# Kernel optimization log

Measured on AMD Instinct MI355X. Metric: run time of the kernel, lower is better.

## Reference

```python
import jax, jax.numpy as jnp
import numpy as np

T, B, F = 256, 256, 128   # seq_len, batch (graph nodes), feature_dim = graph_arch[0]
H1 = 256                  # graph_arch[1]
H = 128                   # graph_arch[-1] == lstm hidden_dim
Q = 4                     # n_qubits bottleneck per gate
TAGS = 32


def setup_inputs() -> dict:
    key = jax.random.key(0)
    ks = jax.random.split(key, 8)
    s = 0.05  # init scale for stability
    return {
        "node_sequences": jax.random.normal(ks[0], (T, B, F), jnp.float32),
        "adj": jax.random.uniform(ks[1], (B, B), jnp.float32),
        "W1": jax.random.normal(ks[2], (F, H1), jnp.float32) * s,
        "b1": jnp.zeros((H1,), jnp.float32),
        "W2": jax.random.normal(ks[3], (H1, H), jnp.float32) * s,
        "b2": jnp.zeros((H,), jnp.float32),
        "Win": jax.random.normal(ks[4], (4, F + H, Q), jnp.float32) * s,   # 4 gates: f,i,g,o
        "b_in": jnp.zeros((4, Q), jnp.float32),
        "Wout": jax.random.normal(ks[5], (4, Q, H), jnp.float32) * s,
        "b_out": jnp.zeros((4, H), jnp.float32),
        "Wtag": jax.random.normal(ks[6], (H, TAGS), jnp.float32) * s,
        "btag": jnp.zeros((TAGS,), jnp.float32),
    }


def reference(node_sequences, adj, W1, b1, W2, b2, Win, b_in, Wout, b_out, Wtag, btag):
    t, b, f = node_sequences.shape
    # per-node feedforward MLP (batched instead of the original per-sample loop)
    flat = node_sequences.reshape(t * b, f)
    a1 = jnp.tanh(flat @ W1 + b1)
    node_states = jnp.tanh(a1 @ W2 + b2).reshape(t, b, -1)   # [T,B,H]
    # fidelity-adjacency aggregation over the node (batch) axis
    aggregated = jnp.einsum('ij,tjf->tif', adj, node_states)  # [T,B,H]

    h_dim = Wout.shape[-1]

    def step(carry, x_t):
        h, c = carry
        v = jnp.concatenate([x_t, h], axis=-1)                       # [B, F+H]
        z = jnp.tanh(jnp.einsum('bv,gvq->gbq', v, Win) + b_in[:, None, :])   # quantum-layer bottleneck [4,B,Q]
        g = jnp.einsum('gbq,gqh->gbh', z, Wout) + b_out[:, None, :]          # [4,B,H]
        f_g = jax.nn.sigmoid(g[0])
        i_g = jax.nn.sigmoid(g[1])
        g_g = jnp.tanh(g[2])
        o_g = jax.nn.sigmoid(g[3])
        c = f_g * c + i_g * g_g
        h = o_g * jnp.tanh(c)
        return (h, c), h

    h0 = jnp.zeros((b, h_dim), node_sequences.dtype)
    c0 = jnp.zeros((b, h_dim), node_sequences.dtype)
    _, lstm_out = jax.lax.scan(step, (h0, c0), aggregated)   # [T,B,H]

    logits = lstm_out @ Wtag + btag                          # [T,B,TAGS]
    return jax.nn.log_softmax(logits, axis=2)
```

## Files before the change

### kernel.cpp

```cpp
#include <hip/hip_runtime.h>
#include <hip/hip_bf16.h>

#define T_DIM 256
#define B_DIM 256
#define F_DIM 128
#define H1_DIM 256
#define H_DIM 128
#define Q_DIM 4
#define TAGS 32
#define TB (T_DIM * B_DIM)

typedef __attribute__((ext_vector_type(8))) short bf16x8;
typedef __attribute__((ext_vector_type(4))) float f32x4;
typedef __attribute__((ext_vector_type(2))) float f32x2;

__device__ __forceinline__ float rcpf(float x) { return __builtin_amdgcn_rcpf(x); }
__device__ __forceinline__ float exp2f_hw(float x) { return __builtin_amdgcn_exp2f(x); }

__device__ __forceinline__ float tanhf_fast(float x) {
    float e = exp2f_hw(2.885390081777927f * x);
    return 1.0f - 2.0f * rcpf(e + 1.0f);
}
__device__ __forceinline__ float sigf(float x) {
    return rcpf(1.0f + exp2f_hw(-1.4426950408889634f * x));
}

__device__ __forceinline__ unsigned short f2bf(float f) {
    __hip_bfloat16 h = __float2bfloat16(f);
    return *reinterpret_cast<unsigned short*>(&h);
}

__device__ __forceinline__ f32x2 pk_mul2(f32x2 a, f32x2 b) {
    f32x2 d;
    asm("v_pk_mul_f32 %0, %1, %2" : "=v"(d) : "v"(a), "v"(b));
    return d;
}
__device__ __forceinline__ f32x2 pk_add2(f32x2 a, f32x2 b) {
    f32x2 d;
    asm("v_pk_add_f32 %0, %1, %2" : "=v"(d) : "v"(a), "v"(b));
    return d;
}
__device__ __forceinline__ f32x2 pk_fma2(f32x2 a, f32x2 b, f32x2 c) {
    f32x2 d;
    asm("v_pk_fma_f32 %0, %1, %2, %3" : "=v"(d) : "v"(a), "v"(b), "v"(c));
    return d;
}

template<int CTRL>
__device__ __forceinline__ float dpp_xadd(float x) {
    int t = __builtin_amdgcn_update_dpp(0, __float_as_int(x), CTRL, 0xF, 0xF, true);
    return x + __int_as_float(t);
}

__global__ __launch_bounds__(256) void prep_kernel(
    const float* __restrict__ W1, const float* __restrict__ W2,
    const float* __restrict__ Win, const float* __restrict__ Wtag,
    unsigned short* __restrict__ W1p, unsigned short* __restrict__ W2p,
    unsigned short* __restrict__ Winxp, unsigned short* __restrict__ Wtagp)
{
    const int gid0 = blockIdx.x * 256 + threadIdx.x;
    const int gstride = gridDim.x * 256;
    for (int idx = gid0; idx < 32768; idx += gstride) {
        int e = idx & 7, l = (idx >> 3) & 63, t2 = idx >> 9;
        int nb = t2 & 15, kk = t2 >> 4;
        int k = kk * 32 + (l >> 4) * 8 + e, n = nb * 16 + (l & 15);
        W1p[idx] = f2bf(W1[k * 256 + n]);
    }
    for (int idx = gid0; idx < 32768; idx += gstride) {
        int e = idx & 7, l = (idx >> 3) & 63, t2 = idx >> 9;
        int nb = t2 & 7, kk = t2 >> 3;
        int k = kk * 32 + (l >> 4) * 8 + e, n = nb * 16 + (l & 15);
        W2p[idx] = f2bf(W2[k * 128 + n]);
    }
    for (int idx = gid0; idx < 2048; idx += gstride) {
        int e = idx & 7, l = (idx >> 3) & 63, kk = idx >> 9;
        int k = kk * 32 + (l >> 4) * 8 + e, o = l & 15;
        Winxp[idx] = f2bf(Win[(o >> 2) * 1024 + k * 4 + (o & 3)]);
    }
    for (int idx = gid0; idx < 4096; idx += gstride) {
        int e = idx & 7, l = (idx >> 3) & 63, t2 = idx >> 9;
        int nt = t2 & 1, kk = t2 >> 1;
        int k = kk * 32 + (l >> 4) * 8 + e, n = nt * 16 + (l & 15);
        Wtagp[idx] = f2bf(Wtag[k * 32 + n]);
    }
}

__global__ __launch_bounds__(256) void mlp_mfma_kernel(
    const float* __restrict__ X, const unsigned short* __restrict__ W1p,
    const float* __restrict__ b1, const unsigned short* __restrict__ W2p,
    const float* __restrict__ b2, const unsigned short* __restrict__ Winxp,
    float* __restrict__ NSP)
{
    __shared__ __align__(16) unsigned short a1_s[64 * 256];
    __shared__ __align__(16) unsigned short xns_s[64 * 128];

    const int tid = threadIdx.x;
    const int w = tid >> 6;
    const int lane = tid & 63;
    const int lr = lane & 15;
    const int lg = lane >> 4;
    const long rowbase = (long)blockIdx.x * 64;

    char* const a1c = (char*)a1_s;
    char* const xnc = (char*)xns_s;

    {
        const int r = tid >> 2;
        const int qc = tid & 3;
        const float4* xg = (const float4*)(X + (rowbase + r) * 128 + qc * 32);
#pragma unroll
        for (int i = 0; i < 4; i++) {
            float4 lo = xg[i * 2], hi = xg[i * 2 + 1];
            bf16x8 v;
            v[0] = (short)f2bf(lo.x); v[1] = (short)f2bf(lo.y);
            v[2] = (short)f2bf(lo.z); v[3] = (short)f2bf(lo.w);
            v[4] = (short)f2bf(hi.x); v[5] = (short)f2bf(hi.y);
            v[6] = (short)f2bf(hi.z); v[7] = (short)f2bf(hi.w);
            int byte = (r * 256 + qc * 64 + i * 16) ^ ((r & 7) << 4);
            *(bf16x8*)(xnc + byte) = v;
        }
    }
    __syncthreads();

    {
        f32x4 acc[4][4];
#pragma unroll
        for (int mi = 0; mi < 4; mi++)
#pragma unroll
            for (int j = 0; j < 4; j++) acc[mi][j] = (f32x4){0.f, 0.f, 0.f, 0.f};

        const bf16x8* w1v = (const bf16x8*)W1p;
#pragma unroll
        for (int kk = 0; kk < 4; kk++) {
            bf16x8 af[4];
#pragma unroll
            for (int mi = 0; mi < 4; mi++) {
                int row = mi * 16 + lr;
                int byte = (row * 256 + kk * 64 + lg * 16) ^ ((row & 7) << 4);
                af[mi] = *(const bf16x8*)(xnc + byte);
            }
            bf16x8 bfv[4];
#pragma unroll
            for (int j = 0; j < 4; j++)
                bfv[j] = w1v[(kk * 16 + (w * 4 + j)) * 64 + lane];
#pragma unroll
            for (int mi = 0; mi < 4; mi++)
#pragma unroll
                for (int j = 0; j < 4; j++)
                    acc[mi][j] = __builtin_amdgcn_mfma_f32_16x16x32_bf16(
                        af[mi], bfv[j], acc[mi][j], 0, 0, 0);
        }

        float b1v[4];
#pragma unroll
        for (int j = 0; j < 4; j++) b1v[j] = b1[(w * 4 + j) * 16 + lr];
#pragma unroll
        for (int mi = 0; mi < 4; mi++)
#pragma unroll
            for (int j = 0; j < 4; j++)
#pragma unroll
                for (int reg = 0; reg < 4; reg++) {
                    int row = mi * 16 + lg * 4 + reg;
                    int col = (w * 4 + j) * 16 + lr;
                    float v = tanhf_fast(acc[mi][j][reg] + b1v[j]);
                    int byte = (row * 512 + col * 2) ^ ((row & 7) << 4);
                    *(unsigned short*)(a1c + byte) = f2bf(v);
                }
    }
    __syncthreads();

    {
        f32x4 acc[4][2];
#pragma unroll
        for (int mi = 0; mi < 4; mi++)
#pragma unroll
            for (int j = 0; j < 2; j++) acc[mi][j] = (f32x4){0.f, 0.f, 0.f, 0.f};

        const bf16x8* w2v = (const bf16x8*)W2p;
#pragma unroll
        for (int kk = 0; kk < 8; kk++) {
            bf16x8 af[4];
#pragma unroll
            for (int mi = 0; mi < 4; mi++) {
                int row = mi * 16 + lr;
                int byte = (row * 512 + kk * 64 + lg * 16) ^ ((row & 7) << 4);
                af[mi] = *(const bf16x8*)(a1c + byte);
            }
            bf16x8 bfv[2];
#pragma unroll
            for (int j = 0; j < 2; j++)
                bfv[j] = w2v[(kk * 8 + (w * 2 + j)) * 64 + lane];
#pragma unroll
            for (int mi = 0; mi < 4; mi++)
#pragma unroll
                for (int j = 0; j < 2; j++)
                    acc[mi][j] = __builtin_amdgcn_mfma_f32_16x16x32_bf16(
                        af[mi], bfv[j], acc[mi][j], 0, 0, 0);
        }

        float b2v[2];
#pragma unroll
        for (int j = 0; j < 2; j++) b2v[j] = b2[(w * 2 + j) * 16 + lr];
#pragma unroll
        for (int mi = 0; mi < 4; mi++)
#pragma unroll
            for (int j = 0; j < 2; j++)
#pragma unroll
                for (int reg = 0; reg < 4; reg++) {
                    int row = mi * 16 + lg * 4 + reg;
                    int col = (w * 2 + j) * 16 + lr;
                    float v = tanhf_fast(acc[mi][j][reg] + b2v[j]);
                    int byte = (row * 256 + col * 2) ^ ((row & 7) << 4);
                    *(unsigned short*)(xnc + byte) = f2bf(v);
                }
    }
    __syncthreads();

    {
        f32x4 acc = (f32x4){0.f, 0.f, 0.f, 0.f};
        const bf16x8* wxv = (const bf16x8*)Winxp;
#pragma unroll
        for (int kk = 0; kk < 4; kk++) {
            int row = w * 16 + lr;
            int byte = (row * 256 + kk * 64 + lg * 16) ^ ((row & 7) << 4);
            bf16x8 af = *(const bf16x8*)(xnc + byte);
            bf16x8 bfv = wxv[kk * 64 + lane];
            acc = __builtin_amdgcn_mfma_f32_16x16x32_bf16(af, bfv, acc, 0, 0, 0);
        }
#pragma unroll
        for (int reg = 0; reg < 4; reg++) {
            int row = w * 16 + lg * 4 + reg;
            NSP[(rowbase + row) * 16 + lr] = acc[reg];
        }
    }
}

__global__ __launch_bounds__(256) void transpose_kernel(
    const float* __restrict__ adj, float* __restrict__ adjT)
{
    __shared__ float tile[32][33];
    const int tid = threadIdx.x;
    const int bx = blockIdx.x & 7, by = blockIdx.x >> 3;
    const int lx = tid & 31, ly = (tid >> 5) * 4;
#pragma unroll
    for (int r = 0; r < 4; r++)
        tile[ly + r][lx] = adj[(long)(by * 32 + ly + r) * 256 + bx * 32 + lx];
    __syncthreads();
#pragma unroll
    for (int r = 0; r < 4; r++)
        adjT[(long)(bx * 32 + ly + r) * 256 + by * 32 + lx] = tile[lx][ly + r];
}

__global__ __launch_bounds__(256) void aggx_kernel(
    const float* __restrict__ adjT, const float* __restrict__ NSP,
    const float* __restrict__ b_in, float* __restrict__ AX)
{
    __shared__ float4 nsp_s[256 * 4];
    const int tid = threadIdx.x;
    const int t = blockIdx.x;
    {
        const float4* g = (const float4*)(NSP + (long)t * 4096);
#pragma unroll
        for (int i = 0; i < 4; i++) nsp_s[tid + i * 256] = g[tid + i * 256];
    }
    __syncthreads();

    float4 acc[4];
#pragma unroll
    for (int p = 0; p < 4; p++) acc[p] = ((const float4*)b_in)[p];

    const float* arow = adjT + tid;
    float a[8], an[8];
#pragma unroll
    for (int m = 0; m < 8; m++) an[m] = arow[m * 256];
    for (int j0 = 0; j0 < 256; j0 += 8) {
#pragma unroll
        for (int m = 0; m < 8; m++) a[m] = an[m];
        if (j0 + 8 < 256) {
#pragma unroll
            for (int m = 0; m < 8; m++) an[m] = arow[(j0 + 8 + m) * 256];
        }
#pragma unroll
        for (int m = 0; m < 8; m++) {
            float av = a[m];
#pragma unroll
            for (int p = 0; p < 4; p++) {
                float4 nv = nsp_s[(j0 + m) * 4 + p];
                acc[p].x += av * nv.x; acc[p].y += av * nv.y;
                acc[p].z += av * nv.z; acc[p].w += av * nv.w;
            }
        }
    }
    float4* out = (float4*)(AX + (long)t * 4096 + tid * 16);
#pragma unroll
    for (int p = 0; p < 4; p++) out[p] = acc[p];
}

__device__ __forceinline__ int hhoff(int row, int inrow) {
    return (row * 512 + inrow) ^ ((row & 7) << 4);
}

__global__ __attribute__((amdgpu_waves_per_eu(1, 1))) __launch_bounds__(64)
void lstm_head_kernel(
    const float* __restrict__ AX, const float* __restrict__ Win,
    const float* __restrict__ Wout, const float* __restrict__ b_out,
    const unsigned short* __restrict__ Wtagp, const float* __restrict__ btag,
    float* __restrict__ OUT)
{
    __shared__ __align__(16) float hh[T_DIM * 128];
    char* const hhc = (char*)hh;

    const int lane = threadIdx.x;
    const int b = blockIdx.x;
    const int o = lane >> 2;
    const int s = lane & 3;
    const int g_o = o >> 2, q_o = o & 3;

    f32x2 wh2[16];
#pragma unroll
    for (int m = 0; m < 8; m++)
#pragma unroll
        for (int p = 0; p < 2; p++) {
            int k0 = m * 16 + s * 4 + p * 2;
            f32x2 v;
            v.x = Win[g_o * 1024 + 512 + k0 * 4 + q_o];
            v.y = Win[g_o * 1024 + 512 + (k0 + 1) * 4 + q_o];
            wh2[m * 2 + p] = v;
        }

    float wo[4][4][2];
    float bo[4][2];
#pragma unroll
    for (int g = 0; g < 4; g++) {
#pragma unroll
        for (int h2 = 0; h2 < 2; h2++) bo[g][h2] = b_out[g * 128 + lane + 64 * h2];
#pragma unroll
        for (int q = 0; q < 4; q++)
#pragma unroll
            for (int h2 = 0; h2 < 2; h2++)
                wo[g][q][h2] = Wout[(g * 4 + q) * 128 + lane + 64 * h2];
    }

    int woffs[8], roffs[8];
#pragma unroll
    for (int sl = 0; sl < 8; sl++) {
        woffs[sl] = (lane * 4) ^ (sl << 4);
        roffs[sl] = (s * 16) ^ ((sl << 4) & 0x30);
    }

    float c0 = 0.f, c1 = 0.f;
    f32x2 hl[8], hx[8];
#pragma unroll
    for (int m = 0; m < 8; m++) { hl[m] = (f32x2){0.f, 0.f}; hx[m] = (f32x2){0.f, 0.f}; }

    const float* axp = AX + (long)b * 16 + o;
    float ax_cur = axp[0];
    float ax_nxt = axp[B_DIM * 16];
    axp += 2 * B_DIM * 16;

    int vbase = 0;
    for (int tb = 0; tb < T_DIM; tb += 8) {
#pragma unroll
        for (int sl = 0; sl < 8; sl++) {
            const int sw6 = (sl << 4) & 0x40;
            f32x2 aA = pk_mul2(hl[0], wh2[0]);
            f32x2 aB = pk_mul2(hl[1], wh2[1]);
            f32x2 aC = pk_mul2(hl[2], wh2[2]);
            f32x2 aD = pk_mul2(hl[3], wh2[3]);
            aA = pk_fma2(hl[4], wh2[4], aA);
            aB = pk_fma2(hl[5], wh2[5], aB);
            aC = pk_fma2(hl[6], wh2[6], aC);
            aD = pk_fma2(hl[7], wh2[7], aD);
            aA = pk_fma2(hx[0], wh2[8],  aA);
            aB = pk_fma2(hx[1], wh2[9],  aB);
            aC = pk_fma2(hx[2], wh2[10], aC);
            aD = pk_fma2(hx[3], wh2[11], aD);
            aA = pk_fma2(hx[4], wh2[12], aA);
            aB = pk_fma2(hx[5], wh2[13], aB);
            aC = pk_fma2(hx[6], wh2[14], aC);
            aD = pk_fma2(hx[7], wh2[15], aD);
            f32x2 sAB = pk_add2(aA, aB);
            f32x2 sCD = pk_add2(aC, aD);
            f32x2 sS  = pk_add2(sAB, sCD);
            float acc = sS.x + sS.y;
            acc = dpp_xadd<0xB1>(acc);
            acc = dpp_xadd<0x4E>(acc);
            float zv = tanhf_fast(acc + ax_cur);

            unsigned zb = __float_as_uint(zv);
            float z[16];
#pragma unroll
            for (int oo = 0; oo < 16; oo++)
                z[oo] = __uint_as_float(__builtin_amdgcn_readlane(zb, oo * 4));

            char* const wp = hhc + (vbase + woffs[sl]);
            const char* const rp = hhc + (vbase + roffs[sl]);

            {
                float gp_f = bo[0][0] + z[0]*wo[0][0][0] + z[1]*wo[0][1][0] + z[2]*wo[0][2][0] + z[3]*wo[0][3][0];
                float gp_i = bo[1][0] + z[4]*wo[1][0][0] + z[5]*wo[1][1][0] + z[6]*wo[1][2][0] + z[7]*wo[1][3][0];
                float gp_g = bo[2][0] + z[8]*wo[2][0][0] + z[9]*wo[2][1][0] + z[10]*wo[2][2][0] + z[11]*wo[2][3][0];
                float gp_o = bo[3][0] + z[12]*wo[3][0][0] + z[13]*wo[3][1][0] + z[14]*wo[3][2][0] + z[15]*wo[3][3][0];
                float fg = sigf(gp_f);
                float ig = sigf(gp_i);
                float gg = tanhf_fast(gp_g);
                float og = sigf(gp_o);
                c0 = fg * c0 + ig * gg;
                float h0 = og * tanhf_fast(c0);
                *(float*)(wp + sl * 512) = h0;
            }
#pragma unroll
            for (int m = 0; m < 4; m++) {
                hl[m * 2]     = *(const f32x2*)(rp + sl * 512 + ((m * 64) ^ sw6));
                hl[m * 2 + 1] = *(const f32x2*)(rp + sl * 512 + ((m * 64) ^ sw6) + 8);
            }

            {
                float gp_f = bo[0][1] + z[0]*wo[0][0][1] + z[1]*wo[0][1][1] + z[2]*wo[0][2][1] + z[3]*wo[0][3][1];
                float gp_i = bo[1][1] + z[4]*wo[1][0][1] + z[5]*wo[1][1][1] + z[6]*wo[1][2][1] + z[7]*wo[1][3][1];
                float gp_g = bo[2][1] + z[8]*wo[2][0][1] + z[9]*wo[2][1][1] + z[10]*wo[2][2][1] + z[11]*wo[2][3][1];
                float gp_o = bo[3][1] + z[12]*wo[3][0][1] + z[13]*wo[3][1][1] + z[14]*wo[3][2][1] + z[15]*wo[3][3][1];
                float fg = sigf(gp_f);
                float ig = sigf(gp_i);
                float gg = tanhf_fast(gp_g);
                float og = sigf(gp_o);
                c1 = fg * c1 + ig * gg;
                float h1 = og * tanhf_fast(c1);
                *(float*)(wp + sl * 512 + 256) = h1;
            }
#pragma unroll
            for (int m = 0; m < 4; m++) {
                hx[m * 2]     = *(const f32x2*)(rp + sl * 512 + 256 + ((m * 64) ^ sw6));
                hx[m * 2 + 1] = *(const f32x2*)(rp + sl * 512 + 256 + ((m * 64) ^ sw6) + 8);
            }

            ax_cur = ax_nxt;
            ax_nxt = *axp;
            axp += B_DIM * 16;
        }
        vbase += 8 * 512;
    }

    const int lr = lane & 15;
    const int lg = lane >> 4;
    const bf16x8* wtv = (const bf16x8*)Wtagp;
    bf16x8 wt[4][2];
#pragma unroll
    for (int kk = 0; kk < 4; kk++)
#pragma unroll
        for (int nt = 0; nt < 2; nt++)
            wt[kk][nt] = wtv[(kk * 2 + nt) * 64 + lane];
    float bt0 = btag[lr], bt1 = btag[16 + lr];

    for (int mi = 0; mi < 16; mi++) {
        f32x4 acc0 = (f32x4){0.f, 0.f, 0.f, 0.f};
        f32x4 acc1 = (f32x4){0.f, 0.f, 0.f, 0.f};
        const int arow = mi * 16 + lr;
#pragma unroll
        for (int kk = 0; kk < 4; kk++) {
            float4 lo = *(const float4*)(hhc + hhoff(arow, kk * 128 + lg * 32));
            float4 hi = *(const float4*)(hhc + hhoff(arow, kk * 128 + lg * 32 + 16));
            bf16x8 af;
            af[0] = (short)f2bf(lo.x); af[1] = (short)f2bf(lo.y);
            af[2] = (short)f2bf(lo.z); af[3] = (short)f2bf(lo.w);
            af[4] = (short)f2bf(hi.x); af[5] = (short)f2bf(hi.y);
            af[6] = (short)f2bf(hi.z); af[7] = (short)f2bf(hi.w);
            acc0 = __builtin_amdgcn_mfma_f32_16x16x32_bf16(af, wt[kk][0], acc0, 0, 0, 0);
            acc1 = __builtin_amdgcn_mfma_f32_16x16x32_bf16(af, wt[kk][1], acc1, 0, 0, 0);
        }
        float s0[4], s1[4], mx[4], se[4];
#pragma unroll
        for (int reg = 0; reg < 4; reg++) {
            s0[reg] = acc0[reg] + bt0;
            s1[reg] = acc1[reg] + bt1;
            float m = fmaxf(s0[reg], s1[reg]);
#pragma unroll
            for (int d = 8; d >= 1; d >>= 1) m = fmaxf(m, __shfl_xor(m, d));
            mx[reg] = m;
            float e = __expf(s0[reg] - m) + __expf(s1[reg] - m);
#pragma unroll
            for (int d = 8; d >= 1; d >>= 1) e += __shfl_xor(e, d);
            se[reg] = __logf(e);
        }
#pragma unroll
        for (int reg = 0; reg < 4; reg++) {
            long t = mi * 16 + lg * 4 + reg;
            long base = (t * B_DIM + b) * 32;
            OUT[base + lr]      = s0[reg] - mx[reg] - se[reg];
            OUT[base + 16 + lr] = s1[reg] - mx[reg] - se[reg];
        }
    }
}

extern "C" void kernel_launch(void* const* d_in, const int* in_sizes, int n_in,
                              void* d_out, int out_size, void* d_ws, size_t ws_size,
                              hipStream_t stream)
{
    const float* X    = (const float*)d_in[0];
    const float* adj  = (const float*)d_in[1];
    const float* W1   = (const float*)d_in[2];
    const float* b1   = (const float*)d_in[3];
    const float* W2   = (const float*)d_in[4];
    const float* b2   = (const float*)d_in[5];
    const float* Win  = (const float*)d_in[6];
    const float* b_in = (const float*)d_in[7];
    const float* Wout = (const float*)d_in[8];
    const float* bout = (const float*)d_in[9];
    const float* Wtag = (const float*)d_in[10];
    const float* btag = (const float*)d_in[11];
    float* OUT = (float*)d_out;

    float* ws = (float*)d_ws;
    float* NSP  = ws;
    float* adjT = ws + 1048576;
    float* AX   = ws + 1114112;
    unsigned short* W1p   = (unsigned short*)(ws + 2162688);
    unsigned short* W2p   = W1p + 32768;
    unsigned short* Winxp = W2p + 32768;
    unsigned short* Wtagp = Winxp + 2048;

    prep_kernel<<<dim3(64), dim3(256), 0, stream>>>(W1, W2, Win, Wtag, W1p, W2p, Winxp, Wtagp);
    mlp_mfma_kernel<<<dim3(TB / 64), dim3(256), 0, stream>>>(X, W1p, b1, W2p, b2, Winxp, NSP);
    transpose_kernel<<<dim3(64), dim3(256), 0, stream>>>(adj, adjT);
    aggx_kernel<<<dim3(256), dim3(256), 0, stream>>>(adjT, NSP, b_in, AX);
    lstm_head_kernel<<<dim3(B_DIM), dim3(64), 0, stream>>>(AX, Win, Wout, bout, Wtagp, btag, OUT);
}
```

Before: 157.2 us.

## Split LSTM recurrence hidden units across two waves with per-step barrier

```diff
diff --git a/kernel.cpp b/kernel.cpp
--- a/kernel.cpp
+++ b/kernel.cpp
@@ -300,7 +300,7 @@
     return (row * 512 + inrow) ^ ((row & 7) << 4);
 }
 
-__global__ __attribute__((amdgpu_waves_per_eu(1, 1))) __launch_bounds__(64)
+__global__ __attribute__((amdgpu_waves_per_eu(1, 1))) __launch_bounds__(128)
 void lstm_head_kernel(
     const float* __restrict__ AX, const float* __restrict__ Win,
     const float* __restrict__ Wout, const float* __restrict__ b_out,
@@ -310,7 +310,9 @@
     __shared__ __align__(16) float hh[T_DIM * 128];
     char* const hhc = (char*)hh;
 
-    const int lane = threadIdx.x;
+    const int tid = threadIdx.x;
+    const int w = tid >> 6;
+    const int lane = tid & 63;
     const int b = blockIdx.x;
     const int o = lane >> 2;
     const int s = lane & 3;
@@ -328,27 +330,25 @@
             wh2[m * 2 + p] = v;
         }
 
-    float wo[4][4][2];
-    float bo[4][2];
+    const int f = w * 64 + lane;
+    float wo[4][4];
+    float bo[4];
 #pragma unroll
     for (int g = 0; g < 4; g++) {
-#pragma unroll
-        for (int h2 = 0; h2 < 2; h2++) bo[g][h2] = b_out[g * 128 + lane + 64 * h2];
+        bo[g] = b_out[g * 128 + f];
 #pragma unroll
         for (int q = 0; q < 4; q++)
-#pragma unroll
-            for (int h2 = 0; h2 < 2; h2++)
-                wo[g][q][h2] = Wout[(g * 4 + q) * 128 + lane + 64 * h2];
+            wo[g][q] = Wout[(g * 4 + q) * 128 + f];
     }
 
     int woffs[8], roffs[8];
 #pragma unroll
     for (int sl = 0; sl < 8; sl++) {
-        woffs[sl] = (lane * 4) ^ (sl << 4);
+        woffs[sl] = ((lane * 4) ^ (sl << 4)) + w * 256;
         roffs[sl] = (s * 16) ^ ((sl << 4) & 0x30);
     }
 
-    float c0 = 0.f, c1 = 0.f;
+    float c = 0.f;
     f32x2 hl[8], hx[8];
 #pragma unroll
     for (int m = 0; m < 8; m++) { hl[m] = (f32x2){0.f, 0.f}; hx[m] = (f32x2){0.f, 0.f}; }
@@ -393,45 +393,34 @@
             for (int oo = 0; oo < 16; oo++)
                 z[oo] = __uint_as_float(__builtin_amdgcn_readlane(zb, oo * 4));
 
-            char* const wp = hhc + (vbase + woffs[sl]);
-            const char* const rp = hhc + (vbase + roffs[sl]);
-
             {
-                float gp_f = bo[0][0] + z[0]*wo[0][0][0] + z[1]*wo[0][1][0] + z[2]*wo[0][2][0] + z[3]*wo[0][3][0];
-                float gp_i = bo[1][0] + z[4]*wo[1][0][0] + z[5]*wo[1][1][0] + z[6]*wo[1][2][0] + z[7]*wo[1][3][0];
-                float gp_g = bo[2][0] + z[8]*wo[2][0][0] + z[9]*wo[2][1][0] + z[10]*wo[2][2][0] + z[11]*wo[2][3][0];
-                float gp_o = bo[3][0] + z[12]*wo[3][0][0] + z[13]*wo[3][1][0] + z[14]*wo[3][2][0] + z[15]*wo[3][3][0];
+                float gp_f = bo[0] + z[0]*wo[0][0] + z[1]*wo[0][1] + z[2]*wo[0][2] + z[3]*wo[0][3];
+                float gp_i = bo[1] + z[4]*wo[1][0] + z[5]*wo[1][1] + z[6]*wo[1][2] + z[7]*wo[1][3];
+                float gp_g = bo[2] + z[8]*wo[2][0] + z[9]*wo[2][1] + z[10]*wo[2][2] + z[11]*wo[2][3];
+                float gp_o = bo[3] + z[12]*wo[3][0] + z[13]*wo[3][1] + z[14]*wo[3][2] + z[15]*wo[3][3];
                 float fg = sigf(gp_f);
                 float ig = sigf(gp_i);
                 float gg = tanhf_fast(gp_g);
                 float og = sigf(gp_o);
-                c0 = fg * c0 + ig * gg;
-                float h0 = og * tanhf_fast(c0);
-                *(float*)(wp + sl * 512) = h0;
+                c = fg * c + ig * gg;
+                float hval = og * tanhf_fast(c);
+                *(float*)(hhc + vbase + sl * 512 + woffs[sl]) = hval;
             }
+
+            __syncthreads();
+
+            const char* const rp = hhc + vbase + sl * 512 + roffs[sl];
 #pragma unroll
             for (int m = 0; m < 4; m++) {
-                hl[m * 2]     = *(const f32x2*)(rp + sl * 512 + ((m * 64) ^ sw6));
-                hl[m * 2 + 1] = *(const f32x2*)(rp + sl * 512 + ((m * 64) ^ sw6) + 8);
+                float4 v4 = *(const float4*)(rp + ((m * 64) ^ sw6));
+                hl[m * 2]     = (f32x2){v4.x, v4.y};
+                hl[m * 2 + 1] = (f32x2){v4.z, v4.w};
             }
-
-            {
-                float gp_f = bo[0][1] + z[0]*wo[0][0][1] + z[1]*wo[0][1][1] + z[2]*wo[0][2][1] + z[3]*wo[0][3][1];
-                float gp_i = bo[1][1] + z[4]*wo[1][0][1] + z[5]*wo[1][1][1] + z[6]*wo[1][2][1] + z[7]*wo[1][3][1];
-                float gp_g = bo[2][1] + z[8]*wo[2][0][1] + z[9]*wo[2][1][1] + z[10]*wo[2][2][1] + z[11]*wo[2][3][1];
-                float gp_o = bo[3][1] + z[12]*wo[3][0][1] + z[13]*wo[3][1][1] + z[14]*wo[3][2][1] + z[15]*wo[3][3][1];
-                float fg = sigf(gp_f);
-                float ig = sigf(gp_i);
-                float gg = tanhf_fast(gp_g);
-                float og = sigf(gp_o);
-                c1 = fg * c1 + ig * gg;
-                float h1 = og * tanhf_fast(c1);
-                *(float*)(wp + sl * 512 + 256) = h1;
-            }
 #pragma unroll
             for (int m = 0; m < 4; m++) {
-                hx[m * 2]     = *(const f32x2*)(rp + sl * 512 + 256 + ((m * 64) ^ sw6));
-                hx[m * 2 + 1] = *(const f32x2*)(rp + sl * 512 + 256 + ((m * 64) ^ sw6) + 8);
+                float4 v4 = *(const float4*)(rp + 256 + ((m * 64) ^ sw6));
+                hx[m * 2]     = (f32x2){v4.x, v4.y};
+                hx[m * 2 + 1] = (f32x2){v4.z, v4.w};
             }
 
             ax_cur = ax_nxt;
@@ -452,7 +441,7 @@
             wt[kk][nt] = wtv[(kk * 2 + nt) * 64 + lane];
     float bt0 = btag[lr], bt1 = btag[16 + lr];
 
-    for (int mi = 0; mi < 16; mi++) {
+    for (int mi = w * 8; mi < w * 8 + 8; mi++) {
         f32x4 acc0 = (f32x4){0.f, 0.f, 0.f, 0.f};
         f32x4 acc1 = (f32x4){0.f, 0.f, 0.f, 0.f};
         const int arow = mi * 16 + lr;
@@ -523,5 +512,5 @@
     mlp_mfma_kernel<<<dim3(TB / 64), dim3(256), 0, stream>>>(X, W1p, b1, W2p, b2, Winxp, NSP);
     transpose_kernel<<<dim3(64), dim3(256), 0, stream>>>(adj, adjT);
     aggx_kernel<<<dim3(256), dim3(256), 0, stream>>>(adjT, NSP, b_in, AX);
-    lstm_head_kernel<<<dim3(B_DIM), dim3(64), 0, stream>>>(AX, Win, Wout, bout, Wtagp, btag, OUT);
-}
+    lstm_head_kernel<<<dim3(B_DIM), dim3(128), 0, stream>>>(AX, Win, Wout, bout, Wtagp, btag, OUT);
+}
```

Result: faster. 139.0 us (-11.6%).
